# Kernel tuning notes

Measured on AMD Instinct MI355X. Metric: run time of the kernel, lower is better.

The kernel has to match this reference:

```python
import jax, jax.numpy as jnp
import numpy as np

EMBD_DIM = 1024
NUM_HEADS = 16
HEAD_DIM = EMBD_DIM // NUM_HEADS


def setup_inputs() -> dict:
    key = jax.random.key(0)
    ks = jax.random.split(key, 9)
    B, S, D = 2, 2048, EMBD_DIM
    scale = 1.0 / np.sqrt(D)
    return {
        "x": jax.random.normal(ks[0], (B, S, D), dtype=jnp.float32),
        "wq": jax.random.normal(ks[1], (D, D), dtype=jnp.float32) * scale,
        "bq": jnp.zeros((D,), dtype=jnp.float32),
        "wk": jax.random.normal(ks[2], (D, D), dtype=jnp.float32) * scale,
        "bk": jnp.zeros((D,), dtype=jnp.float32),
        "wv": jax.random.normal(ks[3], (D, D), dtype=jnp.float32) * scale,
        "bv": jnp.zeros((D,), dtype=jnp.float32),
        "wo": jax.random.normal(ks[4], (D, D), dtype=jnp.float32) * scale,
        "bo": jnp.zeros((D,), dtype=jnp.float32),
    }


def reference(x, wq, bq, wk, bk, wv, bv, wo, bo):
    B, S, D = x.shape
    H, hd = NUM_HEADS, HEAD_DIM
    # projections: weights stored as (in, out) so y = x @ w + b
    q = (x @ wq + bq).reshape(B, S, H, hd).transpose(0, 2, 1, 3)  # [B,H,S,hd]
    k = (x @ wk + bk).reshape(B, S, H, hd).transpose(0, 2, 1, 3)
    v = (x @ wv + bv).reshape(B, S, H, hd).transpose(0, 2, 1, 3)
    scores = jnp.einsum("bhqd,bhkd->bhqk", q, k) / jnp.sqrt(jnp.float32(hd))
    causal = jnp.tril(jnp.ones((S, S), dtype=bool))  # [S,S]
    neg = jnp.finfo(scores.dtype).min
    scores = jnp.where(causal[None, None, :, :], scores, neg)
    attn = jax.nn.softmax(scores, axis=-1)
    out = jnp.einsum("bhqk,bhkd->bhqd", attn, v)  # [B,H,S,hd]
    out = out.transpose(0, 2, 1, 3).reshape(B, S, D)
    return out @ wo + bo
```

## Files before the change

### kernel.cpp

```cpp
#include <hip/hip_runtime.h>
#include <math.h>

#define S_LEN 2048
#define BATCH 2
#define DMODEL 1024
#define NHEADS 16
#define MROWS 4096

typedef short bf8 __attribute__((ext_vector_type(8)));
typedef short bf4 __attribute__((ext_vector_type(4)));
typedef float f32x4 __attribute__((ext_vector_type(4)));
typedef unsigned short u16;

static __device__ inline u16 f2bf(float f) {
    union { float f; unsigned u; } v; v.f = f;
    unsigned r = v.u + 0x7fffu + ((v.u >> 16) & 1u);
    return (u16)(r >> 16);
}

static __device__ inline void load16(const void* g, void* l) {
    __builtin_amdgcn_global_load_lds(
        (const __attribute__((address_space(1))) unsigned int*)g,
        (__attribute__((address_space(3))) unsigned int*)l, 16, 0, 0);
}

__global__ __launch_bounds__(256) void prep_kernel(
    const float* __restrict__ x, u16* __restrict__ xb,
    const float* __restrict__ W0, const float* __restrict__ W1,
    const float* __restrict__ W2, const float* __restrict__ W3,
    u16* __restrict__ wT) {
    const int bx = blockIdx.x, t = threadIdx.x;
    if (bx < 2048) {
        int i = bx * 256 + t;
        const float4* p = (const float4*)x + (size_t)i * 2;
        float4 a = p[0], b = p[1];
        u16 tmp[8] = {f2bf(a.x), f2bf(a.y), f2bf(a.z), f2bf(a.w),
                      f2bf(b.x), f2bf(b.y), f2bf(b.z), f2bf(b.w)};
        ((uint4*)xb)[i] = *(uint4*)tmp;
        return;
    }
    __shared__ u16 Ls[64][65];
    const int id = bx - 2048;
    const int z = id >> 8, rem = id & 255;
    const int n0 = (rem & 15) * 64, k0 = (rem >> 4) * 64;
    const float* W = z == 0 ? W0 : z == 1 ? W1 : z == 2 ? W2 : W3;
    u16* Wt = wT + (size_t)z * 1024 * 1024;
    const int r = t >> 2, c4 = (t & 3) * 16;
    const float* p = W + (size_t)(k0 + r) * 1024 + n0 + c4;
#pragma unroll
    for (int i = 0; i < 16; i += 4) {
        float4 v = *(const float4*)(p + i);
        Ls[r][c4 + i + 0] = f2bf(v.x);
        Ls[r][c4 + i + 1] = f2bf(v.y);
        Ls[r][c4 + i + 2] = f2bf(v.z);
        Ls[r][c4 + i + 3] = f2bf(v.w);
    }
    __syncthreads();
    u16 tmp[16];
#pragma unroll
    for (int i = 0; i < 16; i++) tmp[i] = Ls[c4 + i][r];
    uint4* q = (uint4*)(Wt + (size_t)(n0 + r) * 1024 + k0 + c4);
    q[0] = *(uint4*)tmp;
    q[1] = *(uint4*)(tmp + 8);
}

template <int MODE>
__global__ __launch_bounds__(256) void gemm_mfma(
    const u16* __restrict__ A, const u16* __restrict__ Bt,
    const float* __restrict__ bqp, const float* __restrict__ bkp,
    const float* __restrict__ bvp,
    u16* __restrict__ qout, u16* __restrict__ kout, u16* __restrict__ vtout,
    float* __restrict__ fout, float qscale) {
    __shared__ __align__(16) u16 As[128 * 64];
    __shared__ __align__(16) u16 Bs[128 * 64];

    const int t = threadIdx.x, lane = t & 63, w = t >> 6;
    const int quad = lane >> 4, l16 = lane & 15;
    const int wr = w >> 1, wc = w & 1;
    const int row0 = blockIdx.y * 128, col0 = blockIdx.x * 128;
    const int K = DMODEL;

    const int srow = t >> 3;
    const int ksw = ((t & 7) ^ (srow & 7)) * 8;
    const u16* ag = A + (size_t)(row0 + srow) * K + ksw;
    const u16* bg = Bt + (size_t)(col0 + srow) * K + ksw;
    const int swz = l16 & 7;

    f32x4 acc[4][4] = {};

    u16* lA = As + (size_t)(w * 8) * 64;
    u16* lB = Bs + (size_t)(w * 8) * 64;

    for (int it = 0; it < 16; ++it) {
        if (it) __syncthreads();
        const int k0 = it * 64;
#pragma unroll
        for (int i = 0; i < 4; i++) {
            load16(ag + (size_t)i * 32 * K + k0, lA + i * 32 * 64);
            load16(bg + (size_t)i * 32 * K + k0, lB + i * 32 * 64);
        }
        __syncthreads();
#pragma unroll
        for (int kc = 0; kc < 2; kc++) {
            bf8 xf[4], wf[4];
#pragma unroll
            for (int ni = 0; ni < 4; ni++)
                xf[ni] = *(const bf8*)&As[(wr * 64 + ni * 16 + l16) * 64 +
                                          ((kc * 4 + quad) ^ swz) * 8];
#pragma unroll
            for (int mi = 0; mi < 4; mi++)
                wf[mi] = *(const bf8*)&Bs[(wc * 64 + mi * 16 + l16) * 64 +
                                          ((kc * 4 + quad) ^ swz) * 8];
#pragma unroll
            for (int mi = 0; mi < 4; mi++)
#pragma unroll
                for (int ni = 0; ni < 4; ni++)
                    acc[mi][ni] = __builtin_amdgcn_mfma_f32_16x16x32_bf16(
                        wf[mi], xf[ni], acc[mi][ni], 0, 0, 0);
        }
    }

    const int sect = (col0 + wc * 64) >> 10;
#pragma unroll
    for (int mi = 0; mi < 4; mi++) {
        const int featb = col0 + wc * 64 + mi * 16 + quad * 4;
        float b4[4];
#pragma unroll
        for (int reg = 0; reg < 4; reg++)
            b4[reg] = (MODE == 1 ? bqp : (sect == 0 ? bqp : sect == 1 ? bkp : bvp))
                          [(featb + reg) & 1023];
#pragma unroll
        for (int ni = 0; ni < 4; ni++) {
            const int xrow = row0 + wr * 64 + ni * 16 + l16;
            if (MODE == 1) {
                float4 o;
                o.x = acc[mi][ni][0] + b4[0];
                o.y = acc[mi][ni][1] + b4[1];
                o.z = acc[mi][ni][2] + b4[2];
                o.w = acc[mi][ni][3] + b4[3];
                *(float4*)(fout + (size_t)xrow * 1024 + featb) = o;
            } else {
                const int cf = featb & 1023;
                if (sect == 0) {
                    u16 t4[4];
#pragma unroll
                    for (int reg = 0; reg < 4; reg++)
                        t4[reg] = f2bf((acc[mi][ni][reg] + b4[reg]) * qscale);
                    *(uint2*)(qout + (size_t)xrow * 1024 + cf) = *(uint2*)t4;
                } else if (sect == 1) {
                    u16 t4[4];
#pragma unroll
                    for (int reg = 0; reg < 4; reg++)
                        t4[reg] = f2bf(acc[mi][ni][reg] + b4[reg]);
                    *(uint2*)(kout + (size_t)xrow * 1024 + cf) = *(uint2*)t4;
                } else {
#pragma unroll
                    for (int reg = 0; reg < 4; reg++)
                        vtout[((size_t)(xrow >> 11) * 1024 + cf + reg) * S_LEN +
                              (xrow & 2047)] = f2bf(acc[mi][ni][reg] + b4[reg]);
                }
            }
        }
    }
}

__global__ __launch_bounds__(256) void gemm_oproj(
    const u16* __restrict__ A, const u16* __restrict__ Bt,
    const float* __restrict__ bop, float* __restrict__ fout) {
    __shared__ __align__(16) u16 As[2][64 * 64];
    __shared__ __align__(16) u16 Bs[2][128 * 64];

    const int t = threadIdx.x, lane = t & 63, w = t >> 6;
    const int quad = lane >> 4, l16 = lane & 15;
    const int row0 = blockIdx.y * 64, col0 = blockIdx.x * 128;
    const int K = DMODEL;

    const int lrow = lane >> 3;
    const int koff = ((lane & 7) ^ lrow) * 8;
    const u16* ag = A + (size_t)(row0 + w * 16 + lrow) * K + koff;
    const u16* bg = Bt + (size_t)(col0 + w * 32 + lrow) * K + koff;
    const int swz = l16 & 7;

    f32x4 acc[2][4] = {};

    {
        u16* lA = As[0] + (w * 16) * 64;
        u16* lB = Bs[0] + (w * 32) * 64;
        load16(ag, lA);
        load16(ag + (size_t)8 * K, lA + 512);
#pragma unroll
        for (int d = 0; d < 4; d++)
            load16(bg + (size_t)d * 8 * K, lB + d * 512);
    }

#pragma unroll 2
    for (int it = 0; it < 16; it++) {
        const int buf = it & 1;
        __syncthreads();
        if (it + 1 < 16) {
            const int k0 = (it + 1) * 64;
            u16* lA = As[buf ^ 1] + (w * 16) * 64;
            u16* lB = Bs[buf ^ 1] + (w * 32) * 64;
            load16(ag + k0, lA);
            load16(ag + (size_t)8 * K + k0, lA + 512);
#pragma unroll
            for (int d = 0; d < 4; d++)
                load16(bg + (size_t)d * 8 * K + k0, lB + d * 512);
        }
#pragma unroll
        for (int kc = 0; kc < 2; kc++) {
            bf8 xf[4], wf[2];
#pragma unroll
            for (int ni = 0; ni < 4; ni++)
                xf[ni] = *(const bf8*)&As[buf][(ni * 16 + l16) * 64 +
                                              ((kc * 4 + quad) ^ swz) * 8];
#pragma unroll
            for (int mi = 0; mi < 2; mi++)
                wf[mi] = *(const bf8*)&Bs[buf][(w * 32 + mi * 16 + l16) * 64 +
                                              ((kc * 4 + quad) ^ swz) * 8];
#pragma unroll
            for (int mi = 0; mi < 2; mi++)
#pragma unroll
                for (int ni = 0; ni < 4; ni++)
                    acc[mi][ni] = __builtin_amdgcn_mfma_f32_16x16x32_bf16(
                        wf[mi], xf[ni], acc[mi][ni], 0, 0, 0);
        }
    }

#pragma unroll
    for (int mi = 0; mi < 2; mi++) {
        const int featb = col0 + w * 32 + mi * 16 + quad * 4;
        float b4[4];
#pragma unroll
        for (int reg = 0; reg < 4; reg++)
            b4[reg] = bop[(featb + reg) & 1023];
#pragma unroll
        for (int ni = 0; ni < 4; ni++) {
            const int xrow = row0 + ni * 16 + l16;
            float4 o;
            o.x = acc[mi][ni][0] + b4[0];
            o.y = acc[mi][ni][1] + b4[1];
            o.z = acc[mi][ni][2] + b4[2];
            o.w = acc[mi][ni][3] + b4[3];
            *(float4*)(fout + (size_t)xrow * 1024 + featb) = o;
        }
    }
}

__global__ __launch_bounds__(512, 4) void attn_kernel(
    const u16* __restrict__ Qg, const u16* __restrict__ Kg,
    const u16* __restrict__ Vt, u16* __restrict__ Og) {
    __shared__ __align__(16) u16 LdsF[2 * 16384];

    const int t = threadIdx.x, lane = t & 63, w = t >> 6;
    const int quad = lane >> 4, l16 = lane & 15;
    const int wtile = w >> 2, wq = w & 3;
    const int pi = 15 - blockIdx.y;
    const int bh = blockIdx.x, b = bh >> 4, h = bh & 15;
    const size_t base = (size_t)b * S_LEN * DMODEL + h * 64;
    const size_t vbase = ((size_t)b * 1024 + h * 64) * S_LEN;
    const int swz = (l16 >> 1) & 3;

    const int rK = lane >> 2, cc = lane & 3;
    const int ssS = (rK >> 1) & 3;
    const int chnk = (cc ^ ssS) * 8;
    const u16* src;
    size_t jstr, tstr;
    if (w < 4) {
        src = Kg + base + (size_t)((w & 1) * 64 + rK) * DMODEL +
              (w >> 1) * 32 + chnk;
        jstr = (size_t)16 * DMODEL;
        tstr = (size_t)128 * DMODEL;
    } else {
        const int wv = w - 4;
        src = Vt + vbase + (size_t)rK * S_LEN +
              (wv >> 1) * 64 + (wv & 1) * 32 + chnk;
        jstr = (size_t)16 * S_LEN;
        tstr = (size_t)128;
    }
    const int dstoff = (w * 4) * 512;

#define STAGE(bufsel, tile)                                                    \
    {                                                                          \
        u16* _d = LdsF + (bufsel) * 16384 + dstoff;                            \
        const u16* _s = src + (size_t)(tile) * tstr;                           \
        load16(_s, _d);                                                        \
        load16(_s + jstr, _d + 512);                                           \
        load16(_s + 2 * jstr, _d + 1024);                                      \
        load16(_s + 3 * jstr, _d + 1536);                                      \
    }

    const int niter = pi + 1;
    const int q0 = pi * 128 + wtile * 64;

    bf8 aq[2];
#pragma unroll
    for (int c = 0; c < 2; c++)
        aq[c] = *(const bf8*)(Qg + base +
            (size_t)(q0 + wq * 16 + l16) * DMODEL + c * 32 + quad * 8);

    float lsum = 0.f;
    f32x4 oT[4] = {};

    const int qloc = wtile * 64 + wq * 16 + l16;
    const int qmax = wtile * 64 + wq * 16 + 15;

    STAGE(0, 0)
    __syncthreads();

    for (int kt = 0; kt < niter; kt++) {
        const int cur = kt & 1;
        if (kt + 1 < niter) STAGE(cur ^ 1, kt + 1)
        const u16* KB = LdsF + cur * 16384;
        const u16* VB = KB + 8192;

        f32x4 scv[8] = {};
        __builtin_amdgcn_s_setprio(1);
#pragma unroll
        for (int c = 0; c < 2; c++)
#pragma unroll
            for (int ns = 0; ns < 8; ns++) {
                bf8 ak = *(const bf8*)&KB[(c * 128 + ns * 16 + l16) * 32 +
                                          ((quad ^ swz) * 8)];
                scv[ns] = __builtin_amdgcn_mfma_f32_16x16x32_bf16(
                    ak, aq[c], scv[ns], 0, 0, 0);
            }
        __builtin_amdgcn_s_setprio(0);

        const bool diag = (kt == niter - 1);
#pragma unroll
        for (int ns = 0; ns < 8; ns++) {
            if (diag && ns * 16 > qmax) continue;
            float p[4];
#pragma unroll
            for (int r = 0; r < 4; r++) {
                int key = ns * 16 + quad * 4 + r;
                p[r] = (diag && key > qloc) ? 0.f
                                            : __builtin_amdgcn_exp2f(scv[ns][r]);
                lsum += p[r];
            }
            union { unsigned u[2]; bf4 v; } pk;
            pk.u[0] = (__float_as_uint(p[0]) >> 16) |
                      (__float_as_uint(p[1]) & 0xffff0000u);
            pk.u[1] = (__float_as_uint(p[2]) >> 16) |
                      (__float_as_uint(p[3]) & 0xffff0000u);
            __builtin_amdgcn_s_setprio(1);
#pragma unroll
            for (int ds = 0; ds < 4; ds++) {
                bf4 av = *(const bf4*)&VB[((ns >> 1) * 64 + ds * 16 + l16) * 32 +
                    ((((ns & 1) * 2 + (quad >> 1)) ^ swz) * 8) + (quad & 1) * 4];
                oT[ds] = __builtin_amdgcn_mfma_f32_16x16x16bf16_1k(
                    av, pk.v, oT[ds], 0, 0, 0);
            }
            __builtin_amdgcn_s_setprio(0);
        }
        __syncthreads();
    }
#undef STAGE

    float l = lsum;
    l += __shfl_xor(l, 16, 64);
    l += __shfl_xor(l, 32, 64);
    const float inv = 1.f / l;
    const int qq = q0 + wq * 16 + l16;
#pragma unroll
    for (int ds = 0; ds < 4; ds++) {
        u16 t4[4];
#pragma unroll
        for (int r = 0; r < 4; r++) t4[r] = f2bf(oT[ds][r] * inv);
        *(uint2*)(Og + base + (size_t)qq * DMODEL + ds * 16 + quad * 4) =
            *(uint2*)t4;
    }
}

extern "C" void kernel_launch(void* const* d_in, const int* in_sizes, int n_in,
                              void* d_out, int out_size, void* d_ws, size_t ws_size,
                              hipStream_t stream) {
    const float* x  = (const float*)d_in[0];
    const float* wq = (const float*)d_in[1];
    const float* bq = (const float*)d_in[2];
    const float* wk = (const float*)d_in[3];
    const float* bk = (const float*)d_in[4];
    const float* wv = (const float*)d_in[5];
    const float* bv = (const float*)d_in[6];
    const float* wo = (const float*)d_in[7];
    const float* bo = (const float*)d_in[8];
    float* out = (float*)d_out;

    const size_t E = (size_t)MROWS * DMODEL;
    u16* xb  = (u16*)d_out;
    u16* vt  = xb + E;
    u16* wT  = (u16*)d_ws;
    u16* woT = wT + 3145728;
    u16* qb  = wT + 4194304;
    u16* kb  = qb + E;
    u16* ob  = kb + E;

    dim3 blk(256);
    prep_kernel<<<3072, blk, 0, stream>>>(x, xb, wq, wk, wv, wo, wT);

    gemm_mfma<0><<<dim3(24, 32), blk, 0, stream>>>(
        xb, wT, bq, bk, bv, qb, kb, vt, nullptr, 0.18033688011112042f);

    attn_kernel<<<dim3(BATCH * NHEADS, 16), dim3(512), 0, stream>>>(
        qb, kb, vt, ob);

    gemm_oproj<<<dim3(8, 64), blk, 0, stream>>>(ob, woT, bo, out);
}
```

Before: 182.1 us.

## Rewrite attention kernel with 32x32x16 MFMA, 4-wave blocks and 64-key tiles

Restructures the attention kernel so each block has 4 waves, each owning 32 query rows. Scores and PV use 32x32x16 bf16 MFMA instead of 16x16 variants, over 64-key K/V tiles in a smaller double-buffered LDS with an XOR swizzle. P is packed to bf16 with v_cvt_pk_bf16_f32 (round-to-nearest rather than truncation) and permlane32 swaps to form the B operand. Waves whose queries lie entirely before a key tile skip it. The aim is fewer MFMA and LDS instructions per FLOP and finer causal skipping, at the cost of more sync iterations and changed occupancy.

```diff
diff --git a/kernel.cpp b/kernel.cpp
--- a/kernel.cpp
+++ b/kernel.cpp
@@ -10,6 +10,7 @@
 typedef short bf8 __attribute__((ext_vector_type(8)));
 typedef short bf4 __attribute__((ext_vector_type(4)));
 typedef float f32x4 __attribute__((ext_vector_type(4)));
+typedef float f32x16 __attribute__((ext_vector_type(16)));
 typedef unsigned short u16;
 
 static __device__ inline u16 f2bf(float f) {
@@ -247,63 +248,50 @@
     }
 }
 
-__global__ __launch_bounds__(512, 4) void attn_kernel(
+__global__ __launch_bounds__(256, 2) void attn_kernel(
     const u16* __restrict__ Qg, const u16* __restrict__ Kg,
     const u16* __restrict__ Vt, u16* __restrict__ Og) {
-    __shared__ __align__(16) u16 LdsF[2 * 16384];
+    __shared__ __align__(16) u16 LdsF[2][8192];
 
     const int t = threadIdx.x, lane = t & 63, w = t >> 6;
-    const int quad = lane >> 4, l16 = lane & 15;
-    const int wtile = w >> 2, wq = w & 3;
+    const int l31 = lane & 31, hi = lane >> 5;
     const int pi = 15 - blockIdx.y;
     const int bh = blockIdx.x, b = bh >> 4, h = bh & 15;
     const size_t base = (size_t)b * S_LEN * DMODEL + h * 64;
     const size_t vbase = ((size_t)b * 1024 + h * 64) * S_LEN;
-    const int swz = (l16 >> 1) & 3;
-
-    const int rK = lane >> 2, cc = lane & 3;
-    const int ssS = (rK >> 1) & 3;
-    const int chnk = (cc ^ ssS) * 8;
-    const u16* src;
-    size_t jstr, tstr;
-    if (w < 4) {
-        src = Kg + base + (size_t)((w & 1) * 64 + rK) * DMODEL +
-              (w >> 1) * 32 + chnk;
-        jstr = (size_t)16 * DMODEL;
-        tstr = (size_t)128 * DMODEL;
-    } else {
-        const int wv = w - 4;
-        src = Vt + vbase + (size_t)rK * S_LEN +
-              (wv >> 1) * 64 + (wv & 1) * 32 + chnk;
-        jstr = (size_t)16 * S_LEN;
-        tstr = (size_t)128;
-    }
-    const int dstoff = (w * 4) * 512;
-
-#define STAGE(bufsel, tile)                                                    \
+
+    const int sr8 = lane >> 3, sl = lane & 7;
+    const int r0 = w * 16 + sr8, r1 = w * 16 + 8 + sr8;
+    const int ko0 = ((sl ^ (r0 & 7)) * 8), ko1 = ((sl ^ (r1 & 7)) * 8);
+    const u16* kS0 = Kg + base + (size_t)r0 * DMODEL + ko0;
+    const u16* kS1 = Kg + base + (size_t)r1 * DMODEL + ko1;
+    const u16* vS0 = Vt + vbase + (size_t)r0 * S_LEN + ko0;
+    const u16* vS1 = Vt + vbase + (size_t)r1 * S_LEN + ko1;
+    const int dstK = (w * 16) * 64;
+    const int dstV = 4096 + (w * 16) * 64;
+
+#define STAGE(bs, tile)                                                        \
     {                                                                          \
-        u16* _d = LdsF + (bufsel) * 16384 + dstoff;                            \
-        const u16* _s = src + (size_t)(tile) * tstr;                           \
-        load16(_s, _d);                                                        \
-        load16(_s + jstr, _d + 512);                                           \
-        load16(_s + 2 * jstr, _d + 1024);                                      \
-        load16(_s + 3 * jstr, _d + 1536);                                      \
-    }
-
-    const int niter = pi + 1;
-    const int q0 = pi * 128 + wtile * 64;
-
-    bf8 aq[2];
-#pragma unroll
-    for (int c = 0; c < 2; c++)
-        aq[c] = *(const bf8*)(Qg + base +
-            (size_t)(q0 + wq * 16 + l16) * DMODEL + c * 32 + quad * 8);
+        const size_t kadv = (size_t)(tile) * 64;                               \
+        load16(kS0 + kadv * DMODEL, &LdsF[bs][dstK]);                          \
+        load16(kS1 + kadv * DMODEL, &LdsF[bs][dstK + 512]);                    \
+        load16(vS0 + kadv, &LdsF[bs][dstV]);                                   \
+        load16(vS1 + kadv, &LdsF[bs][dstV + 512]);                             \
+    }
+
+    const int niter = 2 * pi + 2;
+    const int q0 = pi * 128 + w * 32;
+    const int qg = q0 + l31;
+    const int qmax = q0 + 31;
+
+    bf8 aq[4];
+#pragma unroll
+    for (int step = 0; step < 4; step++)
+        aq[step] = *(const bf8*)(Qg + base + (size_t)qg * DMODEL +
+                                 step * 16 + hi * 8);
 
     float lsum = 0.f;
-    f32x4 oT[4] = {};
-
-    const int qloc = wtile * 64 + wq * 16 + l16;
-    const int qmax = wtile * 64 + wq * 16 + 15;
+    f32x16 oT[2] = {};
 
     STAGE(0, 0)
     __syncthreads();
@@ -311,66 +299,86 @@
     for (int kt = 0; kt < niter; kt++) {
         const int cur = kt & 1;
         if (kt + 1 < niter) STAGE(cur ^ 1, kt + 1)
-        const u16* KB = LdsF + cur * 16384;
-        const u16* VB = KB + 8192;
-
-        f32x4 scv[8] = {};
-        __builtin_amdgcn_s_setprio(1);
-#pragma unroll
-        for (int c = 0; c < 2; c++)
-#pragma unroll
-            for (int ns = 0; ns < 8; ns++) {
-                bf8 ak = *(const bf8*)&KB[(c * 128 + ns * 16 + l16) * 32 +
-                                          ((quad ^ swz) * 8)];
-                scv[ns] = __builtin_amdgcn_mfma_f32_16x16x32_bf16(
-                    ak, aq[c], scv[ns], 0, 0, 0);
+        const u16* KB = &LdsF[cur][0];
+        const u16* VB = &LdsF[cur][4096];
+
+        const bool skipw = (kt * 64 > qmax);
+        if (!skipw) {
+            f32x16 scv[2] = {};
+            __builtin_amdgcn_s_setprio(1);
+#pragma unroll
+            for (int step = 0; step < 4; step++)
+#pragma unroll
+                for (int s = 0; s < 2; s++) {
+                    const int key = s * 32 + l31;
+                    bf8 ak = *(const bf8*)&KB[key * 64 +
+                        (((step * 2 + hi) ^ (key & 7)) * 8)];
+                    scv[s] = __builtin_amdgcn_mfma_f32_32x32x16_bf16(
+                        ak, aq[step], scv[s], 0, 0, 0);
+                }
+            __builtin_amdgcn_s_setprio(0);
+
+            const bool masked = (kt * 64 + 63 > q0);
+            const int qthr = masked ? qg : 0x7FFFFFFF;
+            float pf[2][16];
+#pragma unroll
+            for (int s = 0; s < 2; s++) {
+                const int kb2 = kt * 64 + s * 32 + 4 * hi;
+#pragma unroll
+                for (int r = 0; r < 16; r++) {
+                    const int key = kb2 + (r & 3) + 8 * (r >> 2);
+                    float pv = (key > qthr)
+                                   ? 0.f
+                                   : __builtin_amdgcn_exp2f(scv[s][r]);
+                    pf[s][r] = pv;
+                    lsum += pv;
+                }
             }
-        __builtin_amdgcn_s_setprio(0);
-
-        const bool diag = (kt == niter - 1);
-#pragma unroll
-        for (int ns = 0; ns < 8; ns++) {
-            if (diag && ns * 16 > qmax) continue;
-            float p[4];
-#pragma unroll
-            for (int r = 0; r < 4; r++) {
-                int key = ns * 16 + quad * 4 + r;
-                p[r] = (diag && key > qloc) ? 0.f
-                                            : __builtin_amdgcn_exp2f(scv[ns][r]);
-                lsum += p[r];
+#pragma unroll
+            for (int ks = 0; ks < 4; ks++) {
+                const int s = ks >> 1, c = ks & 1;
+                unsigned alo, blo, ahi, bhi;
+                asm("v_cvt_pk_bf16_f32 %0, %1, %2"
+                    : "=v"(alo) : "v"(pf[s][8 * c + 0]), "v"(pf[s][8 * c + 1]));
+                asm("v_cvt_pk_bf16_f32 %0, %1, %2"
+                    : "=v"(blo) : "v"(pf[s][8 * c + 2]), "v"(pf[s][8 * c + 3]));
+                asm("v_cvt_pk_bf16_f32 %0, %1, %2"
+                    : "=v"(ahi) : "v"(pf[s][8 * c + 4]), "v"(pf[s][8 * c + 5]));
+                asm("v_cvt_pk_bf16_f32 %0, %1, %2"
+                    : "=v"(bhi) : "v"(pf[s][8 * c + 6]), "v"(pf[s][8 * c + 7]));
+                asm("v_permlane32_swap_b32 %0, %1" : "+v"(alo), "+v"(ahi));
+                asm("v_permlane32_swap_b32 %0, %1" : "+v"(blo), "+v"(bhi));
+                union { unsigned u[4]; bf8 v; } pk;
+                pk.u[0] = alo; pk.u[1] = blo; pk.u[2] = ahi; pk.u[3] = bhi;
+                __builtin_amdgcn_s_setprio(1);
+#pragma unroll
+                for (int dsub = 0; dsub < 2; dsub++) {
+                    const int d = dsub * 32 + l31;
+                    bf8 av = *(const bf8*)&VB[d * 64 +
+                        (((ks * 2 + hi) ^ (d & 7)) * 8)];
+                    oT[dsub] = __builtin_amdgcn_mfma_f32_32x32x16_bf16(
+                        av, pk.v, oT[dsub], 0, 0, 0);
+                }
+                __builtin_amdgcn_s_setprio(0);
             }
-            union { unsigned u[2]; bf4 v; } pk;
-            pk.u[0] = (__float_as_uint(p[0]) >> 16) |
-                      (__float_as_uint(p[1]) & 0xffff0000u);
-            pk.u[1] = (__float_as_uint(p[2]) >> 16) |
-                      (__float_as_uint(p[3]) & 0xffff0000u);
-            __builtin_amdgcn_s_setprio(1);
-#pragma unroll
-            for (int ds = 0; ds < 4; ds++) {
-                bf4 av = *(const bf4*)&VB[((ns >> 1) * 64 + ds * 16 + l16) * 32 +
-                    ((((ns & 1) * 2 + (quad >> 1)) ^ swz) * 8) + (quad & 1) * 4];
-                oT[ds] = __builtin_amdgcn_mfma_f32_16x16x16bf16_1k(
-                    av, pk.v, oT[ds], 0, 0, 0);
-            }
-            __builtin_amdgcn_s_setprio(0);
         }
         __syncthreads();
     }
 #undef STAGE
 
-    float l = lsum;
-    l += __shfl_xor(l, 16, 64);
-    l += __shfl_xor(l, 32, 64);
-    const float inv = 1.f / l;
-    const int qq = q0 + wq * 16 + l16;
-#pragma unroll
-    for (int ds = 0; ds < 4; ds++) {
-        u16 t4[4];
-#pragma unroll
-        for (int r = 0; r < 4; r++) t4[r] = f2bf(oT[ds][r] * inv);
-        *(uint2*)(Og + base + (size_t)qq * DMODEL + ds * 16 + quad * 4) =
-            *(uint2*)t4;
-    }
+    lsum += __shfl_xor(lsum, 32, 64);
+    const float inv = 1.f / lsum;
+#pragma unroll
+    for (int dsub = 0; dsub < 2; dsub++)
+#pragma unroll
+        for (int g = 0; g < 4; g++) {
+            u16 t4[4];
+#pragma unroll
+            for (int m = 0; m < 4; m++)
+                t4[m] = f2bf(oT[dsub][g * 4 + m] * inv);
+            *(uint2*)(Og + base + (size_t)qg * DMODEL + dsub * 32 + g * 8 +
+                      hi * 4) = *(uint2*)t4;
+        }
 }
 
 extern "C" void kernel_launch(void* const* d_in, const int* in_sizes, int n_in,
@@ -402,7 +410,7 @@
     gemm_mfma<0><<<dim3(24, 32), blk, 0, stream>>>(
         xb, wT, bq, bk, bv, qb, kb, vt, nullptr, 0.18033688011112042f);
 
-    attn_kernel<<<dim3(BATCH * NHEADS, 16), dim3(512), 0, stream>>>(
+    attn_kernel<<<dim3(BATCH * NHEADS, 16), blk, 0, stream>>>(
         qb, kb, vt, ob);
 
     gemm_oproj<<<dim3(8, 64), blk, 0, stream>>>(ob, woT, bo, out);
```

New measurement: 189.5 us. 4.1% more time.
